# Kernel tuning notes

Measured on AMD Instinct MI355X. Metric: run time of the kernel, lower is better.

The kernel has to match this reference:

```python
import jax, jax.numpy as jnp
import numpy as np

NEG_INF = -1e30


def setup_inputs() -> dict:
    key = jax.random.key(0)
    kx, km, kq, kk, kv, ko = jax.random.split(key, 6)
    B, D, L = 2, 1024, 2048
    H, DK = 16, 64
    x = jax.random.normal(kx, (B, D, L), dtype=jnp.float32)
    mask = (jax.random.uniform(km, (B, L)) < 0.9).astype(jnp.float32)
    # per-head projection weights, stacked: (H, D, DK); output proj (D, H*DK)==(D, D)
    sq = 1.0 / np.sqrt(D)
    Wq = jax.random.normal(kq, (H, D, DK), dtype=jnp.float32) * sq
    Wk = jax.random.normal(kk, (H, D, DK), dtype=jnp.float32) * sq
    Wv = jax.random.normal(kv, (H, D, DK), dtype=jnp.float32) * sq
    Wo = jax.random.normal(ko, (D, H * DK), dtype=jnp.float32) * sq
    return {"x": x, "mask": mask, "Wq": Wq, "Wk": Wk, "Wv": Wv, "Wo": Wo}


def reference(x, mask, Wq, Wk, Wv, Wo):
    # x: (B, D, L); original transposes to (B, L, D)
    B, D, L = x.shape
    H, _, DK = Wq.shape
    xt = jnp.transpose(x, (0, 2, 1))  # (B, L, D)
    q = jnp.einsum('bld,hdk->bhlk', xt, Wq)
    k = jnp.einsum('bld,hdk->bhlk', xt, Wk)
    v = jnp.einsum('bld,hdk->bhlk', xt, Wv)
    scores = jnp.einsum('bhlk,bhmk->bhlm', q, k) * (1.0 / np.sqrt(DK))
    # masked log-softmax over keys (hmask), squad-style: mask*logit + (1-mask)*-1e30
    hmask = mask[:, None, None, :]  # (B,1,1,Lk)
    masked = hmask * scores + (1.0 - hmask) * NEG_INF
    logp = jax.nn.log_softmax(masked, axis=-1)
    # second softmax over the log-probs, then multiplicative vmask on query dim
    p = jax.nn.softmax(logp, axis=-1) * mask[:, None, :, None]
    heads = jnp.einsum('bhlm,bhmk->bhlk', p, v)  # (B,H,L,DK)
    head = jnp.transpose(heads, (0, 2, 1, 3)).reshape(B, L, H * DK)
    out = jnp.einsum('ble,de->bld', head, Wo)  # matmul(head, Wo) with Wo (D, H*DK)... 
    # NOTE: torch.matmul(head, Wo) treats Wo as (H*DK_in, D_out) only if square; here
    # Wo is (D, H*DK) with D == H*DK, and torch contracts head's last dim with Wo's FIRST dim:
    out = head @ Wo  # (B, L, H*DK) @ (D, H*DK) requires D==H*DK; contracts dim 0 of Wo
    return jnp.transpose(out, (0, 2, 1))  # (B, D, L)


if __name__ == "__main__":
    print(reference(**setup_inputs()).shape)
```

## Files before the change

### kernel.cpp

```cpp
#include <hip/hip_runtime.h>
#include <hip/hip_bf16.h>

typedef unsigned short u16;
typedef unsigned int u32;
typedef unsigned long long u64;
typedef short s8v __attribute__((ext_vector_type(8)));
typedef __bf16 bfv8 __attribute__((ext_vector_type(8)));
typedef float f4 __attribute__((ext_vector_type(4)));
typedef float f16v __attribute__((ext_vector_type(16)));

static constexpr int B = 2, D = 1024, L = 2048, H = 16, DK = 64, E = 1024;
static constexpr float QSCALE = 0.125f * 1.44269504088896340736f;
static constexpr float SMB = -16.0f;
static constexpr float MASKB = -12000.0f;

#define DEV __device__ __forceinline__

DEV u16 f2bf(float f) {
  unsigned int u = __float_as_uint(f);
  u += 0x7FFFu + ((u >> 16) & 1u);
  return (u16)(u >> 16);
}
DEV float fexp2(float x) { return __builtin_amdgcn_exp2f(x); }
DEV u32 pkbf(float a, float b) {
  __hip_bfloat162 h = __float22bfloat162_rn(float2{a, b});
  u32 r;
  __builtin_memcpy(&r, &h, 4);
  return r;
}
DEV int kperm32(int k) {
  return (k & ~12) | ((k & 4) << 1) | ((k & 8) >> 1);
}

#define GLD_LDS16(gp, lp)                                                     \
  __builtin_amdgcn_global_load_lds(                                           \
      (const __attribute__((address_space(1))) void*)(gp),                    \
      (__attribute__((address_space(3))) void*)(lp), 16, 0, 0)

__global__ __launch_bounds__(256) void k_prep(
    const float* __restrict__ x, const float* __restrict__ Wq,
    const float* __restrict__ Wk, const float* __restrict__ Wv,
    const float* __restrict__ Wo, u16* __restrict__ xt, u16* __restrict__ Wt,
    u16* __restrict__ WoT) {
  __shared__ u16 t[64][67];
  const int tid = threadIdx.x;
  const int g = blockIdx.x;
  const float* src;
  u16* dst;
  int sld, dld;
  if (g < 1024) {
    const int b = g >> 9, dt = (g >> 5) & 15, lt = g & 31;
    src = x + ((size_t)b * D + dt * 64) * L + lt * 64;
    sld = L;
    dst = xt + ((size_t)b * L + lt * 64) * D + dt * 64;
    dld = D;
  } else if (g < 1792) {
    const int u = g - 1024;
    const int w = u >> 8, h = (u >> 4) & 15, dt = u & 15;
    const float* Ws = (w == 0) ? Wq : ((w == 1) ? Wk : Wv);
    src = Ws + ((size_t)h * D + dt * 64) * DK;
    sld = DK;
    dst = Wt + ((size_t)(w * H + h) * DK) * D + dt * 64;
    dld = D;
  } else {
    const int v = g - 1792;
    const int et = v >> 4, dt = v & 15;
    src = Wo + ((size_t)et * 64) * D + dt * 64;
    sld = D;
    dst = WoT + ((size_t)dt * 64) * E + et * 64;
    dld = E;
  }
  const int r = tid >> 2, c16 = (tid & 3) * 16;
#pragma unroll
  for (int j = 0; j < 16; j += 4) {
    const f4 v4 = *(const f4*)(src + (size_t)r * sld + c16 + j);
    t[r][c16 + j]     = f2bf(v4[0]);
    t[r][c16 + j + 1] = f2bf(v4[1]);
    t[r][c16 + j + 2] = f2bf(v4[2]);
    t[r][c16 + j + 3] = f2bf(v4[3]);
  }
  __syncthreads();
  s8v o0, o1;
#pragma unroll
  for (int i = 0; i < 8; ++i) {
    o0[i] = (short)t[c16 + i][r];
    o1[i] = (short)t[c16 + 8 + i][r];
  }
  *(s8v*)(dst + (size_t)r * dld + c16)     = o0;
  *(s8v*)(dst + (size_t)r * dld + c16 + 8) = o1;
}

template <int AR>
DEV void gemm_tile(const u16* __restrict__ A, const u16* __restrict__ Bt,
                   int arow0, int brow0, u16* As, u16* Bs,
                   f4 (&acc)[AR / 32][4]) {
  const int tid = threadIdx.x;
  const int wid = tid >> 6, lane = tid & 63;
  const int q = lane >> 4, ln = lane & 15;
  const int wr = wid >> 1, wc = wid & 1;
  const int lrow = lane >> 3;
  const int lc = (lane & 7) ^ lrow;
  const int f0 = (q ^ (ln & 7)) * 8;
  const int f1 = ((q + 4) ^ (ln & 7)) * 8;
  constexpr int MT = AR / 32;

  for (int k0 = 0; k0 < 1024; k0 += 64) {
    __syncthreads();
#pragma unroll
    for (int j = 0; j < AR / 32; ++j) {
      const int rb = wid * (AR / 4) + j * 8;
      GLD_LDS16(A + (size_t)(arow0 + rb + lrow) * 1024 + k0 + lc * 8,
                As + rb * 64);
    }
#pragma unroll
    for (int j = 0; j < 4; ++j) {
      const int rb = wid * 32 + j * 8;
      GLD_LDS16(Bt + (size_t)(brow0 + rb + lrow) * 1024 + k0 + lc * 8,
                Bs + rb * 64);
    }
    __syncthreads();
#pragma unroll
    for (int ks = 0; ks < 2; ++ks) {
      const int fc = ks ? f1 : f0;
      bfv8 af[MT], bf[4];
#pragma unroll
      for (int mt = 0; mt < MT; ++mt)
        af[mt] = *(const bfv8*)(As + (wr * (AR / 2) + mt * 16 + ln) * 64 + fc);
#pragma unroll
      for (int nt = 0; nt < 4; ++nt)
        bf[nt] = *(const bfv8*)(Bs + (wc * 64 + nt * 16 + ln) * 64 + fc);
#pragma unroll
      for (int mt = 0; mt < MT; ++mt)
#pragma unroll
        for (int nt = 0; nt < 4; ++nt)
          acc[mt][nt] = __builtin_amdgcn_mfma_f32_16x16x32_bf16(
              af[mt], bf[nt], acc[mt][nt], 0, 0, 0);
    }
  }
}

__global__ __launch_bounds__(256, 3) void k_qkvg(
    const u16* __restrict__ xt, const u16* __restrict__ Wt,
    u16* __restrict__ Q, u16* __restrict__ K, u16* __restrict__ Vt) {
  __shared__ u16 As[128 * 64];
  __shared__ u16 Bs[128 * 64];
  const int bm = blockIdx.x, bn = blockIdx.y;
  f4 acc[4][4];
#pragma unroll
  for (int mt = 0; mt < 4; ++mt)
#pragma unroll
    for (int nt = 0; nt < 4; ++nt) acc[mt][nt] = (f4){0.f, 0.f, 0.f, 0.f};
  gemm_tile<128>(xt, Wt, bm * 128, bn * 128, As, Bs, acc);

  const int tid = threadIdx.x, wid = tid >> 6, lane = tid & 63;
  const int q = lane >> 4, ln = lane & 15;
  const int wr = wid >> 1, wc = wid & 1;
  const int h2 = bn * 2 + wc;
  const int wsel = h2 >> 4, h = h2 & 15;
  const int b = bm >> 4;
  const int lbase = (bm & 15) * 128 + wr * 64;
  if (wsel == 0) {
    u16* dst = Q + (size_t)(b * H + h) * L * DK;
#pragma unroll
    for (int mt = 0; mt < 4; ++mt)
#pragma unroll
      for (int nt = 0; nt < 4; ++nt)
#pragma unroll
        for (int r = 0; r < 4; ++r)
          dst[(size_t)(lbase + mt * 16 + q * 4 + r) * DK + nt * 16 + ln] =
              f2bf(acc[mt][nt][r] * QSCALE);
  } else if (wsel == 1) {
    u16* dst = K + (size_t)(b * H + h) * L * DK;
#pragma unroll
    for (int mt = 0; mt < 4; ++mt)
#pragma unroll
      for (int nt = 0; nt < 4; ++nt)
#pragma unroll
        for (int r = 0; r < 4; ++r)
          dst[(size_t)(lbase + mt * 16 + q * 4 + r) * DK + nt * 16 + ln] =
              f2bf(acc[mt][nt][r]);
  } else {
    u16* dst = Vt + (size_t)(b * H + h) * DK * L;
#pragma unroll
    for (int mt = 0; mt < 4; ++mt)
#pragma unroll
      for (int nt = 0; nt < 4; ++nt) {
        const u64 pk = (u64)pkbf(acc[mt][nt][0], acc[mt][nt][1]) |
                       ((u64)pkbf(acc[mt][nt][2], acc[mt][nt][3]) << 32);
        *(u64*)(dst + (size_t)(nt * 16 + ln) * L + lbase + mt * 16 + q * 4) =
            pk;
      }
  }
}

__global__ __launch_bounds__(256, 2) void k_attn(
    const u16* __restrict__ Q, const u16* __restrict__ K,
    const u16* __restrict__ Vt, const float* __restrict__ mask,
    u16* __restrict__ Hd) {
  __shared__ u16 kt[2][128 * 64];
  __shared__ u16 vt[2][2][64 * 64];
  __shared__ __align__(16) float mb[L];
  const int h = blockIdx.x, lt = blockIdx.y, b = blockIdx.z;
  const int tid = threadIdx.x;
  const int w = tid >> 6, lane = tid & 63;
  const int l5 = lane & 31, hi = lane >> 5;
  for (int i = tid; i < L; i += 256)
    mb[i] = (mask[(size_t)b * L + i] != 0.0f) ? SMB : MASKB;

  const int bh = b * H + h;
  const u16* Qp = Q + (size_t)bh * L * DK;
  const u16* Kp = K + (size_t)bh * L * DK;
  const u16* Vp = Vt + (size_t)bh * DK * L;
  const int lq = lt * 128 + w * 32;

  bfv8 qf[4];
#pragma unroll
  for (int st = 0; st < 4; ++st)
    qf[st] = *(const bfv8*)(Qp + (size_t)(lq + l5) * DK + st * 16 + hi * 8);

  const int lrow = lane >> 3;
  const int lc = (lane & 7) ^ lrow;
  const int x7 = lane & 7;
  int kpr[4];
#pragma unroll
  for (int j = 0; j < 4; ++j) kpr[j] = kperm32(w * 32 + j * 8 + lrow);

  auto stage = [&](int m0, int bufi) {
#pragma unroll
    for (int j = 0; j < 4; ++j) {
      GLD_LDS16(Kp + (size_t)(m0 + kpr[j]) * DK + lc * 8,
                &kt[bufi][(w * 32 + j * 8) * 64]);
    }
#pragma unroll
    for (int kh = 0; kh < 2; ++kh)
#pragma unroll
      for (int j = 0; j < 2; ++j) {
        const int fr = w * 16 + j * 8 + lrow;
        GLD_LDS16(Vp + (size_t)fr * L + m0 + kh * 64 + lc * 8,
                  &vt[bufi][kh][(w * 16 + j * 8) * 64]);
      }
  };

  f16v ot[2];
#pragma unroll
  for (int dt = 0; dt < 2; ++dt)
#pragma unroll
    for (int i = 0; i < 16; ++i) ot[dt][i] = 0.f;
  float lp = 0.f;

  stage(0, 0);
  for (int it = 0; it < L / 128; ++it) {
    const int m0 = it * 128;
    __syncthreads();
    if (it + 1 < L / 128) stage(m0 + 128, (it + 1) & 1);
    const int cur = it & 1;
    const u16* ktc = &kt[cur][0];
#pragma unroll
    for (int s = 0; s < 4; ++s) {
      union {
        f4 q[4];
        f16v v;
      } ai;
#pragma unroll
      for (int rq = 0; rq < 4; ++rq)
        ai.q[rq] = *(const f4*)(mb + m0 + s * 32 + (rq >> 1) * 16 + hi * 8 +
                                (rq & 1) * 4);
      f16v a = ai.v;
#pragma unroll
      for (int st = 0; st < 4; ++st) {
        const bfv8 kf = *(const bfv8*)(ktc + (s * 32 + l5) * 64 +
                                       ((st * 2 + hi) ^ x7) * 8);
        a = __builtin_amdgcn_mfma_f32_32x32x16_bf16(kf, qf[st], a, 0, 0, 0);
      }
      float p[16];
#pragma unroll
      for (int i = 0; i < 16; ++i) p[i] = fexp2(a[i]);
      const float t0 = (p[0] + p[1]) + (p[2] + p[3]);
      const float t1 = (p[4] + p[5]) + (p[6] + p[7]);
      const float t2 = (p[8] + p[9]) + (p[10] + p[11]);
      const float t3 = (p[12] + p[13]) + (p[14] + p[15]);
      lp += (t0 + t1) + (t2 + t3);
      union {
        u32 w4[4];
        bfv8 v;
      } pb[2];
#pragma unroll
      for (int g = 0; g < 2; ++g)
#pragma unroll
        for (int k2 = 0; k2 < 4; ++k2)
          pb[g].w4[k2] = pkbf(p[g * 8 + k2 * 2], p[g * 8 + k2 * 2 + 1]);
#pragma unroll
      for (int g = 0; g < 2; ++g) {
        const int kg = s * 2 + g;
        const u16* vtc = &vt[cur][kg >> 2][0];
        const int cb = (((kg & 3) * 2 + hi) ^ x7) * 8;
#pragma unroll
        for (int dt = 0; dt < 2; ++dt) {
          const bfv8 av = *(const bfv8*)(vtc + (dt * 32 + l5) * 64 + cb);
          ot[dt] = __builtin_amdgcn_mfma_f32_32x32x16_bf16(av, pb[g].v,
                                                           ot[dt], 0, 0, 0);
        }
      }
    }
  }
  lp += __shfl_xor(lp, 32);
  const float linv = (mb[lq + l5] > -100.0f) ? (1.0f / lp) : 0.0f;
#pragma unroll
  for (int dt = 0; dt < 2; ++dt)
#pragma unroll
    for (int rq = 0; rq < 4; ++rq) {
      const u64 pk =
          (u64)pkbf(ot[dt][rq * 4 + 0] * linv, ot[dt][rq * 4 + 1] * linv) |
          ((u64)pkbf(ot[dt][rq * 4 + 2] * linv, ot[dt][rq * 4 + 3] * linv)
           << 32);
      *(u64*)(Hd + (size_t)(b * L + lq + l5) * E + h * DK + dt * 32 + rq * 8 +
              hi * 4) = pk;
    }
}

__global__ __launch_bounds__(256, 2) void k_projg(const u16* __restrict__ WoT,
                                                  const u16* __restrict__ Hd,
                                                  float* __restrict__ out) {
  __shared__ u16 As[64 * 64];
  __shared__ u16 Bs[128 * 64];
  const int bm = blockIdx.x, bn = blockIdx.y;
  f4 acc[2][4];
#pragma unroll
  for (int mt = 0; mt < 2; ++mt)
#pragma unroll
    for (int nt = 0; nt < 4; ++nt) acc[mt][nt] = (f4){0.f, 0.f, 0.f, 0.f};
  gemm_tile<64>(WoT, Hd, bm * 64, bn * 128, As, Bs, acc);

  const int tid = threadIdx.x, wid = tid >> 6, lane = tid & 63;
  const int q = lane >> 4, ln = lane & 15;
  const int wr = wid >> 1, wc = wid & 1;
#pragma unroll
  for (int mt = 0; mt < 2; ++mt)
#pragma unroll
    for (int nt = 0; nt < 4; ++nt)
#pragma unroll
      for (int r = 0; r < 4; ++r) {
        const int d = bm * 64 + wr * 32 + mt * 16 + q * 4 + r;
        const int n = bn * 128 + wc * 64 + nt * 16 + ln;
        const int bb = n >> 11, l = n & 2047;
        out[((size_t)(bb * D + d)) * L + l] = acc[mt][nt][r];
      }
}

extern "C" void kernel_launch(void* const* d_in, const int* in_sizes, int n_in,
                              void* d_out, int out_size, void* d_ws,
                              size_t ws_size, hipStream_t stream) {
  const float* x    = (const float*)d_in[0];
  const float* mask = (const float*)d_in[1];
  const float* Wq   = (const float*)d_in[2];
  const float* Wk   = (const float*)d_in[3];
  const float* Wv   = (const float*)d_in[4];
  const float* Wo   = (const float*)d_in[5];
  u16* ws = (u16*)d_ws;
  u16* Qws  = ws;
  u16* Kws  = ws + 4194304;
  u16* Vtws = ws + 8388608;
  u16* WoTw = ws + 12582912;
  u16* Wtws = ws + 13631488;
  u16* xtws = ws + 16777216;
  u16* Hdws = ws + 16777216;

  k_prep<<<2048, 256, 0, stream>>>(x, Wq, Wk, Wv, Wo, xtws, Wtws, WoTw);
  k_qkvg<<<dim3(32, 24), 256, 0, stream>>>(xtws, Wtws, Qws, Kws, Vtws);
  k_attn<<<dim3(16, 16, 2), 256, 0, stream>>>(Qws, Kws, Vtws, mask, Hdws);
  k_projg<<<dim3(16, 32), 256, 0, stream>>>(WoTw, Hdws, (float*)d_out);
}
```

Baseline: 182.3 us.

## Split attention key tiles across wave pairs and reduce partial outputs in LDS

The attention kernel moves to 512 threads per block. Each pair of waves now shares one 32-row query strip, and each wave handles half of every 128-key tile, which doubles the waves available to hide MFMA and exp latency. Partial output accumulators and row sums from the second wave are combined through LDS at the end, and s_setprio is raised around the MFMA sections. The cost is an extra block-level reduction and syncs, plus higher register pressure under the 4-blocks launch bound.

```diff
diff --git a/kernel.cpp b/kernel.cpp
--- a/kernel.cpp
+++ b/kernel.cpp
@@ -193,7 +193,7 @@
   }
 }
 
-__global__ __launch_bounds__(256, 2) void k_attn(
+__global__ __launch_bounds__(512, 4) void k_attn(
     const u16* __restrict__ Q, const u16* __restrict__ K,
     const u16* __restrict__ Vt, const float* __restrict__ mask,
     u16* __restrict__ Hd) {
@@ -204,14 +204,15 @@
   const int tid = threadIdx.x;
   const int w = tid >> 6, lane = tid & 63;
   const int l5 = lane & 31, hi = lane >> 5;
-  for (int i = tid; i < L; i += 256)
+  const int wq = w >> 1, wk = w & 1;
+  for (int i = tid; i < L; i += 512)
     mb[i] = (mask[(size_t)b * L + i] != 0.0f) ? SMB : MASKB;
 
   const int bh = b * H + h;
   const u16* Qp = Q + (size_t)bh * L * DK;
   const u16* Kp = K + (size_t)bh * L * DK;
   const u16* Vp = Vt + (size_t)bh * DK * L;
-  const int lq = lt * 128 + w * 32;
+  const int lq = lt * 128 + wq * 32;
 
   bfv8 qf[4];
 #pragma unroll
@@ -221,31 +222,33 @@
   const int lrow = lane >> 3;
   const int lc = (lane & 7) ^ lrow;
   const int x7 = lane & 7;
-  int kpr[4];
-#pragma unroll
-  for (int j = 0; j < 4; ++j) kpr[j] = kperm32(w * 32 + j * 8 + lrow);
+  int kpr[2];
+#pragma unroll
+  for (int j = 0; j < 2; ++j) kpr[j] = kperm32(w * 16 + j * 8 + lrow);
 
   auto stage = [&](int m0, int bufi) {
 #pragma unroll
-    for (int j = 0; j < 4; ++j) {
+    for (int j = 0; j < 2; ++j) {
       GLD_LDS16(Kp + (size_t)(m0 + kpr[j]) * DK + lc * 8,
-                &kt[bufi][(w * 32 + j * 8) * 64]);
-    }
-#pragma unroll
-    for (int kh = 0; kh < 2; ++kh)
-#pragma unroll
-      for (int j = 0; j < 2; ++j) {
-        const int fr = w * 16 + j * 8 + lrow;
-        GLD_LDS16(Vp + (size_t)fr * L + m0 + kh * 64 + lc * 8,
-                  &vt[bufi][kh][(w * 16 + j * 8) * 64]);
-      }
+                &kt[bufi][(w * 16 + j * 8) * 64]);
+    }
+    const int kh = w >> 2, wv = w & 3;
+#pragma unroll
+    for (int j = 0; j < 2; ++j) {
+      const int fr = wv * 16 + j * 8 + lrow;
+      GLD_LDS16(Vp + (size_t)fr * L + m0 + kh * 64 + lc * 8,
+                &vt[bufi][kh][(wv * 16 + j * 8) * 64]);
+    }
   };
 
-  f16v ot[2];
+  union {
+    f16v v;
+    f4 q[4];
+  } ot[2];
 #pragma unroll
   for (int dt = 0; dt < 2; ++dt)
 #pragma unroll
-    for (int i = 0; i < 16; ++i) ot[dt][i] = 0.f;
+    for (int i = 0; i < 16; ++i) ot[dt].v[i] = 0.f;
   float lp = 0.f;
 
   stage(0, 0);
@@ -255,8 +258,10 @@
     if (it + 1 < L / 128) stage(m0 + 128, (it + 1) & 1);
     const int cur = it & 1;
     const u16* ktc = &kt[cur][0];
-#pragma unroll
-    for (int s = 0; s < 4; ++s) {
+    const u16* vtc = &vt[cur][wk][0];
+#pragma unroll
+    for (int s2 = 0; s2 < 2; ++s2) {
+      const int s = wk * 2 + s2;
       union {
         f4 q[4];
         f16v v;
@@ -266,12 +271,14 @@
         ai.q[rq] = *(const f4*)(mb + m0 + s * 32 + (rq >> 1) * 16 + hi * 8 +
                                 (rq & 1) * 4);
       f16v a = ai.v;
+      __builtin_amdgcn_s_setprio(1);
 #pragma unroll
       for (int st = 0; st < 4; ++st) {
         const bfv8 kf = *(const bfv8*)(ktc + (s * 32 + l5) * 64 +
                                        ((st * 2 + hi) ^ x7) * 8);
         a = __builtin_amdgcn_mfma_f32_32x32x16_bf16(kf, qf[st], a, 0, 0, 0);
       }
+      __builtin_amdgcn_s_setprio(0);
       float p[16];
 #pragma unroll
       for (int i = 0; i < 16; ++i) p[i] = fexp2(a[i]);
@@ -289,33 +296,57 @@
 #pragma unroll
         for (int k2 = 0; k2 < 4; ++k2)
           pb[g].w4[k2] = pkbf(p[g * 8 + k2 * 2], p[g * 8 + k2 * 2 + 1]);
+      __builtin_amdgcn_s_setprio(1);
 #pragma unroll
       for (int g = 0; g < 2; ++g) {
         const int kg = s * 2 + g;
-        const u16* vtc = &vt[cur][kg >> 2][0];
         const int cb = (((kg & 3) * 2 + hi) ^ x7) * 8;
 #pragma unroll
         for (int dt = 0; dt < 2; ++dt) {
           const bfv8 av = *(const bfv8*)(vtc + (dt * 32 + l5) * 64 + cb);
-          ot[dt] = __builtin_amdgcn_mfma_f32_32x32x16_bf16(av, pb[g].v,
-                                                           ot[dt], 0, 0, 0);
+          ot[dt].v = __builtin_amdgcn_mfma_f32_32x32x16_bf16(
+              av, pb[g].v, ot[dt].v, 0, 0, 0);
         }
       }
+      __builtin_amdgcn_s_setprio(0);
     }
   }
   lp += __shfl_xor(lp, 32);
-  const float linv = (mb[lq + l5] > -100.0f) ? (1.0f / lp) : 0.0f;
-#pragma unroll
-  for (int dt = 0; dt < 2; ++dt)
-#pragma unroll
-    for (int rq = 0; rq < 4; ++rq) {
-      const u64 pk =
-          (u64)pkbf(ot[dt][rq * 4 + 0] * linv, ot[dt][rq * 4 + 1] * linv) |
-          ((u64)pkbf(ot[dt][rq * 4 + 2] * linv, ot[dt][rq * 4 + 3] * linv)
-           << 32);
-      *(u64*)(Hd + (size_t)(b * L + lq + l5) * E + h * DK + dt * 32 + rq * 8 +
-              hi * 4) = pk;
-    }
+  __syncthreads();
+  float* sOt = (float*)&kt[0][0];
+  float* sLp = (float*)&vt[0][0][0];
+  if (wk) {
+#pragma unroll
+    for (int dt = 0; dt < 2; ++dt)
+#pragma unroll
+      for (int rq = 0; rq < 4; ++rq)
+        *(f4*)(sOt + ((((wq * 2 + dt) * 4 + rq) * 64) + lane) * 4) =
+            ot[dt].q[rq];
+    sLp[wq * 64 + lane] = lp;
+  }
+  __syncthreads();
+  if (!wk) {
+#pragma unroll
+    for (int dt = 0; dt < 2; ++dt)
+#pragma unroll
+      for (int rq = 0; rq < 4; ++rq)
+        ot[dt].q[rq] +=
+            *(const f4*)(sOt + ((((wq * 2 + dt) * 4 + rq) * 64) + lane) * 4);
+    lp += sLp[wq * 64 + lane];
+    const float linv = (mb[lq + l5] > -100.0f) ? (1.0f / lp) : 0.0f;
+#pragma unroll
+    for (int dt = 0; dt < 2; ++dt)
+#pragma unroll
+      for (int rq = 0; rq < 4; ++rq) {
+        const u64 pk = (u64)pkbf(ot[dt].v[rq * 4 + 0] * linv,
+                                 ot[dt].v[rq * 4 + 1] * linv) |
+                       ((u64)pkbf(ot[dt].v[rq * 4 + 2] * linv,
+                                  ot[dt].v[rq * 4 + 3] * linv)
+                        << 32);
+        *(u64*)(Hd + (size_t)(b * L + lq + l5) * E + h * DK + dt * 32 +
+                rq * 8 + hi * 4) = pk;
+      }
+  }
 }
 
 __global__ __launch_bounds__(256, 2) void k_projg(const u16* __restrict__ WoT,
@@ -367,6 +398,6 @@
 
   k_prep<<<2048, 256, 0, stream>>>(x, Wq, Wk, Wv, Wo, xtws, Wtws, WoTw);
   k_qkvg<<<dim3(32, 24), 256, 0, stream>>>(xtws, Wtws, Qws, Kws, Vtws);
-  k_attn<<<dim3(16, 16, 2), 256, 0, stream>>>(Qws, Kws, Vtws, mask, Hdws);
+  k_attn<<<dim3(16, 16, 2), 512, 0, stream>>>(Qws, Kws, Vtws, mask, Hdws);
   k_projg<<<dim3(16, 32), 256, 0, stream>>>(WoTw, Hdws, (float*)d_out);
 }
```

Result: faster. 177.9 us (-2.4%).
